# Kernel optimization log

Hardware: AMD Instinct MI355X
Metric: run time of the kernel (lower is better)

Reference implementation:

```python
import jax, jax.numpy as jnp
import numpy as np

NF = 64      # feature channels of h
K = 3        # dynamic filter spatial size (padding=1 in source implies k=3)
FACTOR = 4   # pixel-unshuffle factor


def shuffle_down(x, f):
    # torch pixel_unshuffle: (B,C,H*f,W*f) -> (B,C*f*f,H,W)
    B, C, H, W = x.shape
    x = x.reshape(B, C, H // f, f, W // f, f)
    x = x.transpose(0, 1, 3, 5, 2, 4)
    return x.reshape(B, C * f * f, H // f, W // f)


def _patches3x3(x):
    # x: (B,C,H,W) -> (B,C,9,H,W): zero-padded 3x3 neighborhoods, row-major taps,
    # identical to the identity-filter grouped conv (im2col) in the source.
    H, W = x.shape[-2], x.shape[-1]
    xp = jnp.pad(x, ((0, 0), (0, 0), (1, 1), (1, 1)))
    shifts = [xp[:, :, dy:dy + H, dx:dx + W] for dy in range(K) for dx in range(K)]
    return jnp.stack(shifts, axis=2)


def setup_inputs() -> dict:
    key = jax.random.key(0)
    k1, k2, k3, k4 = jax.random.split(key, 4)
    B, H, W = 2, 256, 256
    h = jax.random.normal(k1, (B, NF, H, W), dtype=jnp.float32)
    i_t = jax.random.normal(k2, (B, 3, H * FACTOR, W * FACTOR), dtype=jnp.float32)
    conv_w = jax.random.normal(k3, (K * K, 3 * FACTOR ** 2, K, K), dtype=jnp.float32) * 0.05
    conv_b = jax.random.normal(k4, (K * K,), dtype=jnp.float32) * 0.05
    return {"h": h, "i_t": i_t, "conv_w": conv_w, "conv_b": conv_b}


def reference(h, i_t, conv_w, conv_b):
    # predict per-pixel 3x3 filters from the shuffled-down guidance frame
    x = shuffle_down(i_t, FACTOR)  # (B, 48, H, W)
    f = jax.lax.conv_general_dilated(
        x, conv_w, window_strides=(1, 1), padding=((1, 1), (1, 1)),
        dimension_numbers=("NCHW", "OIHW", "NCHW"))
    filters = jax.nn.relu(f + conv_b[None, :, None, None])  # (B, 9, H, W)

    # dynamic per-pixel conv: same 3x3 filter applied to every channel of h
    patches = _patches3x3(h)  # (B, nf, 9, H, W)
    out = jnp.einsum("bcfhw,bfhw->bchw", patches, filters)  # (B, nf, H, W)
    return out
```

## Files before the change

### kernel.cpp

```cpp
#include <hip/hip_runtime.h>

#define TILE 16
#define HSZ 256
#define WSZ 256
#define NFC 64
#define PLANE (HSZ * WSZ)

typedef __attribute__((ext_vector_type(8))) short short8;
typedef __attribute__((ext_vector_type(4))) float f32x4;

__device__ inline unsigned short f2bf(float f) {
    unsigned u = __builtin_bit_cast(unsigned, f);
    return (unsigned short)((u + 0x7fffu + ((u >> 16) & 1u)) >> 16);
}

__global__ void prep_wfrag(const float* __restrict__ wbuf,
                           unsigned short* __restrict__ wfragG)
{
    const int kb   = blockIdx.x;
    const int lane = threadIdx.x;
    const int l15  = lane & 15;
    const int kg   = lane >> 4;
    unsigned short v8[8];
#pragma unroll
    for (int j = 0; j < 8; ++j) {
        const int k = kb * 32 + kg * 8 + j;
        float w = 0.f;
        if (k < 432 && l15 < 9) {
            const int kk = k / 48;
            const int ic = k - kk * 48;
            w = wbuf[l15 * 432 + ic * 9 + kk];
        }
        v8[j] = f2bf(w);
    }
    unsigned short* p = wfragG + (size_t)kb * 512 + lane * 8;
    *(ushort4*)(p)     = ushort4{v8[0], v8[1], v8[2], v8[3]};
    *(ushort4*)(p + 4) = ushort4{v8[4], v8[5], v8[6], v8[7]};
}

__global__ __launch_bounds__(128) void filter_conv_mfma2(
    const float* __restrict__ i_t,
    const unsigned short* __restrict__ wfragG,
    const float* __restrict__ bias,
    float* __restrict__ fbuf)
{
    __shared__ __align__(16) unsigned short xs[180 * 48];

    const int tid  = threadIdx.x;
    const int X0 = blockIdx.x * 16;
    const int Y0 = blockIdx.y * 8;
    const int b  = blockIdx.z;
    const int lane = tid & 63;
    const int l15  = tid & 15;
    const int kg   = (tid >> 4) & 3;
    const int wv   = tid >> 6;

    const float bv = (l15 < 9) ? bias[l15] : 0.f;
    const float* itb = i_t + (size_t)b * 3 * (PLANE * 16);

    {
        float4 lreg[17]; int sdst[17];
#pragma unroll
        for (int k = 0; k < 17; ++k) {
            const int v = tid + 128 * k;
            const int sp = v / 12, t = v - sp * 12;
            const int c3 = t >> 2, fy = t & 3;
            const int ly = sp / 18, lx = sp - ly * 18;
            const int Y = Y0 - 1 + ly, X = X0 - 1 + lx;
            float4 val = make_float4(0.f, 0.f, 0.f, 0.f);
            if (v < 2160 && (unsigned)Y < HSZ && (unsigned)X < WSZ)
                val = *(const float4*)(itb + ((size_t)c3 * 1024 + (4 * Y + fy)) * 1024 + 4 * X);
            lreg[k] = val;
            sdst[k] = (v < 2160) ? (sp * 48 + t * 4) : -1;
        }
#pragma unroll
        for (int k = 0; k < 17; ++k) {
            if (sdst[k] >= 0) {
                ushort4 u{f2bf(lreg[k].x), f2bf(lreg[k].y), f2bf(lreg[k].z), f2bf(lreg[k].w)};
                *(ushort4*)(xs + sdst[k]) = u;
            }
        }
    }

    short8 wf[14];
#pragma unroll
    for (int kb = 0; kb < 14; ++kb)
        wf[kb] = *(const short8*)(wfragG + (size_t)kb * 512 + lane * 8);

    __syncthreads();

    f32x4 acc0 = {0.f, 0.f, 0.f, 0.f}, acc1 = acc0, acc2 = acc0, acc3 = acc0;
#pragma unroll
    for (int kb = 0; kb < 14; ++kb) {
        const int k0 = kb * 32 + kg * 8;
        int off = 0;
        if (k0 < 432) {
            const int kk  = k0 / 48;
            const int ic0 = k0 - kk * 48;
            const int ky  = kk / 3;
            const int kx  = kk - 3 * ky;
            off = ((wv * 4 + ky) * 18 + l15 + kx) * 48 + ic0;
        }
        short8 a0 = *(const short8*)(xs + off);
        short8 a1 = *(const short8*)(xs + off + 864);
        short8 a2 = *(const short8*)(xs + off + 1728);
        short8 a3 = *(const short8*)(xs + off + 2592);
        acc0 = __builtin_amdgcn_mfma_f32_16x16x32_bf16(a0, wf[kb], acc0, 0, 0, 0);
        acc1 = __builtin_amdgcn_mfma_f32_16x16x32_bf16(a1, wf[kb], acc1, 0, 0, 0);
        acc2 = __builtin_amdgcn_mfma_f32_16x16x32_bf16(a2, wf[kb], acc2, 0, 0, 0);
        acc3 = __builtin_amdgcn_mfma_f32_16x16x32_bf16(a3, wf[kb], acc3, 0, 0, 0);
    }

    __syncthreads();
    float* lf = (float*)xs;
    if (l15 < 9) {
#pragma unroll
        for (int i = 0; i < 4; ++i) {
            const int py = wv * 4 + i;
            f32x4 A = (i == 0) ? acc0 : (i == 1) ? acc1 : (i == 2) ? acc2 : acc3;
#pragma unroll
            for (int r = 0; r < 4; ++r) {
                const int px = kg * 4 + r;
                lf[(py * 16 + px) * 12 + l15] = fmaxf(A[r] + bv, 0.f);
            }
        }
    }
    __syncthreads();
    float* fb = fbuf + (size_t)b * PLANE * 12;
#pragma unroll
    for (int k = 0; k < 3; ++k) {
        const int v = tid + 128 * k;
        const int row = v / 48, off = v - row * 48;
        *(float4*)(fb + ((size_t)(Y0 + row) * WSZ + X0) * 12 + off * 4) =
            *(const float4*)(lf + v * 4);
    }
}

__global__ __launch_bounds__(256, 4) void dyn_apply4(
    const float* __restrict__ hbuf,
    const float* __restrict__ fbuf,
    float* __restrict__ out)
{
    __shared__ __align__(16) float hs[8 * 18 * 40];

    const int tid  = threadIdx.x;
    const int pq   = tid & 7;
    const int py   = (tid >> 3) & 15;
    const int c_lo = tid >> 7;
    const int cg = blockIdx.x & 7;
    const int X0 = (blockIdx.x >> 3) * 32;
    const int Y0 = blockIdx.y * TILE;
    const int b  = blockIdx.z;

    float flt[4][9];
    {
        const float* fb = fbuf + ((size_t)b * PLANE + (size_t)(Y0 + py) * WSZ + X0 + pq * 4) * 12;
#pragma unroll
        for (int j = 0; j < 4; ++j) {
            float4 f0 = *(const float4*)(fb + j * 12);
            float4 f1 = *(const float4*)(fb + j * 12 + 4);
            float  f8 = fb[j * 12 + 8];
            flt[j][0] = f0.x; flt[j][1] = f0.y; flt[j][2] = f0.z; flt[j][3] = f0.w;
            flt[j][4] = f1.x; flt[j][5] = f1.y; flt[j][6] = f1.z; flt[j][7] = f1.w;
            flt[j][8] = f8;
        }
    }

    const float* hp = hbuf + ((size_t)b * NFC + cg * 8) * PLANE;
    {
        float rv[20]; int dst[20];
#pragma unroll
        for (int k = 0; k < 20; ++k) {
            const int v = tid + 256 * k;
            const int c = v / 612;
            const int r = v - c * 612;
            const int row = r / 34, l = r - row * 34;
            const int Y = Y0 - 1 + row;
            const int X = X0 - 1 + l;
            float val = 0.f;
            if (v < 4896 && (unsigned)Y < HSZ && (unsigned)X < WSZ)
                val = hp[(size_t)c * PLANE + (size_t)Y * WSZ + X];
            rv[k] = val;
            dst[k] = (v < 4896) ? (c * 720 + row * 40 + 3 + l) : -1;
        }
#pragma unroll
        for (int k = 0; k < 20; ++k)
            if (dst[k] >= 0) hs[dst[k]] = rv[k];
    }
    __syncthreads();

    float a[4][4];
#pragma unroll
    for (int cc = 0; cc < 4; ++cc)
#pragma unroll
        for (int j = 0; j < 4; ++j) a[cc][j] = 0.f;

#pragma unroll
    for (int cc = 0; cc < 4; ++cc) {
        const float* pl = hs + (c_lo + 2 * cc) * 720;
#pragma unroll
        for (int ky = 0; ky < 3; ++ky) {
            const float* rp = pl + (py + ky) * 40 + pq * 4;
            float4 w0 = *(const float4*)rp;
            float4 w1 = *(const float4*)(rp + 4);
            float  w8 = rp[8];
            const float vs[9] = {w0.x, w0.y, w0.z, w0.w, w1.x, w1.y, w1.z, w1.w, w8};
#pragma unroll
            for (int kx = 0; kx < 3; ++kx)
#pragma unroll
                for (int j = 0; j < 4; ++j)
                    a[cc][j] = fmaf(vs[3 + kx + j], flt[j][ky * 3 + kx], a[cc][j]);
        }
    }

#pragma unroll
    for (int cc = 0; cc < 4; ++cc) {
        const int ch = cg * 8 + c_lo + 2 * cc;
        *(float4*)(out + ((size_t)b * NFC + ch) * PLANE
                       + (size_t)(Y0 + py) * WSZ + X0 + pq * 4)
            = make_float4(a[cc][0], a[cc][1], a[cc][2], a[cc][3]);
    }
}

__global__ void filter_conv_mfma(const float* __restrict__ i_t,
                                 const float* __restrict__ wbuf,
                                 const float* __restrict__ bias,
                                 float* __restrict__ fbuf)
{
    __shared__ __align__(16) unsigned short xs[324 * 56];

    const int tid = threadIdx.x;
    const int X0 = blockIdx.x * TILE;
    const int Y0 = blockIdx.y * TILE;
    const int b  = blockIdx.z;
    const int l15 = tid & 15;
    const int kg  = (tid >> 4) & 3;
    const int wv  = tid >> 6;

    float* wsh = (float*)xs;
    for (int i = tid; i < 3888; i += 256) wsh[i] = wbuf[i];
    __syncthreads();

    short8 wfrag[14];
#pragma unroll
    for (int kb = 0; kb < 14; ++kb) {
#pragma unroll
        for (int j = 0; j < 8; ++j) {
            const int k = kb * 32 + kg * 8 + j;
            float w = 0.f;
            if (k < 432 && l15 < 9) {
                const int kk = k / 48;
                const int ic = k - kk * 48;
                w = wsh[l15 * 432 + ic * 9 + kk];
            }
            wfrag[kb][j] = (short)f2bf(w);
        }
    }
    const float bv = (l15 < 9) ? bias[l15] : 0.f;
    __syncthreads();

    const float* itb = i_t + (size_t)b * 3 * (PLANE * 16);
    for (int v = tid; v < 3888; v += 256) {
        const int sp = v / 12;
        const int t  = v - sp * 12;
        const int c3 = t >> 2, fy = t & 3;
        const int ly = sp / 18, lx = sp - ly * 18;
        const int Y = Y0 - 1 + ly, X = X0 - 1 + lx;
        float4 val = make_float4(0.f, 0.f, 0.f, 0.f);
        if (Y >= 0 && Y < HSZ && X >= 0 && X < WSZ)
            val = *(const float4*)(itb + ((size_t)c3 * 1024 + (4 * Y + fy)) * 1024 + 4 * X);
        ushort4 u;
        u.x = f2bf(val.x); u.y = f2bf(val.y); u.z = f2bf(val.z); u.w = f2bf(val.w);
        *(ushort4*)(xs + sp * 56 + t * 4) = u;
    }
    __syncthreads();

    f32x4 acc0 = {0.f, 0.f, 0.f, 0.f}, acc1 = acc0, acc2 = acc0, acc3 = acc0;
#pragma unroll
    for (int kb = 0; kb < 14; ++kb) {
        const int k0 = kb * 32 + kg * 8;
        int off = 0;
        if (k0 < 432) {
            const int kk  = k0 / 48;
            const int ic0 = k0 - kk * 48;
            const int ky  = kk / 3;
            const int kx  = kk - 3 * ky;
            off = ((wv * 4 + ky) * 18 + l15 + kx) * 56 + ic0;
        }
        short8 a0 = *(const short8*)(xs + off);
        short8 a1 = *(const short8*)(xs + off + 1008);
        short8 a2 = *(const short8*)(xs + off + 2016);
        short8 a3 = *(const short8*)(xs + off + 3024);
        acc0 = __builtin_amdgcn_mfma_f32_16x16x32_bf16(a0, wfrag[kb], acc0, 0, 0, 0);
        acc1 = __builtin_amdgcn_mfma_f32_16x16x32_bf16(a1, wfrag[kb], acc1, 0, 0, 0);
        acc2 = __builtin_amdgcn_mfma_f32_16x16x32_bf16(a2, wfrag[kb], acc2, 0, 0, 0);
        acc3 = __builtin_amdgcn_mfma_f32_16x16x32_bf16(a3, wfrag[kb], acc3, 0, 0, 0);
    }

    if (l15 < 9) {
        float* fb = fbuf + (size_t)b * PLANE * 12;
#pragma unroll
        for (int i = 0; i < 4; ++i) {
            const int py = wv * 4 + i;
            f32x4 A = (i == 0) ? acc0 : (i == 1) ? acc1 : (i == 2) ? acc2 : acc3;
#pragma unroll
            for (int r = 0; r < 4; ++r) {
                const int px = kg * 4 + r;
                fb[((size_t)(Y0 + py) * WSZ + X0 + px) * 12 + l15] = fmaxf(A[r] + bv, 0.f);
            }
        }
    }
}

__global__ __launch_bounds__(256, 2) void fused_dynfilter(
    const float* __restrict__ hbuf,
    const float* __restrict__ i_t,
    const float* __restrict__ wbuf,
    const float* __restrict__ bias,
    float* __restrict__ out)
{
    __shared__ __align__(16) float smem[15552];
    float4* xs4 = (float4*)smem;

    const int tid = threadIdx.x;
    const int px = tid & 15;
    const int py = tid >> 4;
    const int X0 = blockIdx.x * TILE;
    const int Y0 = blockIdx.y * TILE;
    const int b  = blockIdx.z;

    const float* itb = i_t + (size_t)b * 3 * 1024 * 1024;
    for (int v = tid; v < 3888; v += 256) {
        int sp = v / 12;
        int t  = v - sp * 12;
        int c3 = t >> 2, fy = t & 3;
        int ly = sp / 18, lx = sp - ly * 18;
        int Y = Y0 - 1 + ly, X = X0 - 1 + lx;
        float4 val = make_float4(0.f, 0.f, 0.f, 0.f);
        if (Y >= 0 && Y < HSZ && X >= 0 && X < WSZ)
            val = *(const float4*)(itb + ((size_t)c3 * 1024 + (4 * Y + fy)) * 1024 + 4 * X);
        xs4[t * 324 + sp] = val;
    }
    __syncthreads();

    float acc[9];
#pragma unroll
    for (int oc = 0; oc < 9; ++oc) acc[oc] = bias[oc];

#pragma unroll 1
    for (int ky = 0; ky < 3; ++ky)
#pragma unroll 1
        for (int kx = 0; kx < 3; ++kx) {
            const int sp = (py + ky) * 18 + (px + kx);
            const int kk = ky * 3 + kx;
#pragma unroll
            for (int ic4 = 0; ic4 < 12; ++ic4) {
                float4 v = xs4[ic4 * 324 + sp];
                const int chb = ((ic4 >> 2) << 4) + ((ic4 & 3) << 2);
                const float* wp = wbuf + (size_t)chb * 9 + kk;
                const float vv[4] = {v.x, v.y, v.z, v.w};
#pragma unroll
                for (int j = 0; j < 4; ++j)
#pragma unroll
                    for (int oc = 0; oc < 9; ++oc)
                        acc[oc] = fmaf(vv[j], wp[j * 9 + (size_t)oc * 432], acc[oc]);
            }
        }

    float flt[9];
#pragma unroll
    for (int oc = 0; oc < 9; ++oc) flt[oc] = fmaxf(acc[oc], 0.f);

    float4* hs4 = (float4*)smem;
#pragma unroll 1
    for (int cg = 0; cg < 16; ++cg) {
        __syncthreads();
        const float* hp = hbuf + ((size_t)b * NFC + cg * 4) * PLANE;
        for (int idx = tid; idx < 1296; idx += 256) {
            int c  = idx / 324;
            int sp = idx - c * 324;
            int ly = sp / 18, lx = sp - ly * 18;
            int Y = Y0 - 1 + ly, X = X0 - 1 + lx;
            float vv = 0.f;
            if (Y >= 0 && Y < HSZ && X >= 0 && X < WSZ)
                vv = hp[(size_t)c * PLANE + (size_t)Y * WSZ + X];
            smem[sp * 4 + c] = vv;
        }
        __syncthreads();

        float s0 = 0.f, s1 = 0.f, s2 = 0.f, s3 = 0.f;
#pragma unroll
        for (int ky = 0; ky < 3; ++ky)
#pragma unroll
            for (int kx = 0; kx < 3; ++kx) {
                float4 v = hs4[(py + ky) * 18 + (px + kx)];
                float f = flt[ky * 3 + kx];
                s0 = fmaf(v.x, f, s0);
                s1 = fmaf(v.y, f, s1);
                s2 = fmaf(v.z, f, s2);
                s3 = fmaf(v.w, f, s3);
            }
        size_t o = (((size_t)b * NFC + cg * 4) * HSZ + (Y0 + py)) * WSZ + (X0 + px);
        out[o]                     = s0;
        out[o + (size_t)PLANE]     = s1;
        out[o + (size_t)2 * PLANE] = s2;
        out[o + (size_t)3 * PLANE] = s3;
    }
}

extern "C" void kernel_launch(void* const* d_in, const int* in_sizes, int n_in,
                              void* d_out, int out_size, void* d_ws, size_t ws_size,
                              hipStream_t stream) {
    const float* h      = (const float*)d_in[0];
    const float* i_t    = (const float*)d_in[1];
    const float* conv_w = (const float*)d_in[2];
    const float* conv_b = (const float*)d_in[3];
    float* out = (float*)d_out;

    const int B = in_sizes[0] / (NFC * PLANE);
    const size_t fbuf_sz  = (size_t)B * PLANE * 12 * sizeof(float);
    const size_t wfrag_sz = 14 * 512 * sizeof(unsigned short);

    if (ws_size >= fbuf_sz + wfrag_sz) {
        float* fbuf = (float*)d_ws;
        unsigned short* wfragG = (unsigned short*)((char*)d_ws + fbuf_sz);
        prep_wfrag<<<dim3(14), 64, 0, stream>>>(conv_w, wfragG);
        dim3 g1(WSZ / 16, HSZ / 8, B);
        filter_conv_mfma2<<<g1, 128, 0, stream>>>(i_t, wfragG, conv_b, fbuf);
        dim3 g2((WSZ / 32) * 8, HSZ / TILE, B);
        dyn_apply4<<<g2, 256, 0, stream>>>(h, fbuf, out);
    } else if (ws_size >= fbuf_sz) {
        float* fbuf = (float*)d_ws;
        dim3 g1(WSZ / TILE, HSZ / TILE, B);
        filter_conv_mfma<<<g1, 256, 0, stream>>>(i_t, conv_w, conv_b, fbuf);
        dim3 g2((WSZ / 32) * 8, HSZ / TILE, B);
        dyn_apply4<<<g2, 256, 0, stream>>>(h, fbuf, out);
    } else {
        dim3 grid(WSZ / TILE, HSZ / TILE, B);
        fused_dynfilter<<<grid, 256, 0, stream>>>(h, i_t, conv_w, conv_b, out);
    }
}
```

Measured before the change: 137.7 us.

## Store filters planar, vectorize halo loads, widen filter-conv blocks to 256 threads

The intermediate filter buffer changes from a per-pixel 12-float interleaved layout to nine planar channel arrays. This shrinks it from 12 to 9 floats per pixel, so the apply kernel reads filters as float4 per channel. The apply kernel's halo load of h now uses float4 global loads with an aligned 4-float left margin instead of scalar loads. The filter conv uses 256 threads with two MFMA row tiles per wave instead of four, giving more waves per block and fewer registers per thread. It also drops the unused intermediate fallback path. The apply kernel now over-fetches some halo columns, and the filter conv writes in smaller pieces.

```diff
diff --git a/kernel.cpp b/kernel.cpp
--- a/kernel.cpp
+++ b/kernel.cpp
@@ -38,11 +38,11 @@
     *(ushort4*)(p + 4) = ushort4{v8[4], v8[5], v8[6], v8[7]};
 }
 
-__global__ __launch_bounds__(128) void filter_conv_mfma2(
+__global__ __launch_bounds__(256) void filter_conv_mfma3(
     const float* __restrict__ i_t,
     const unsigned short* __restrict__ wfragG,
     const float* __restrict__ bias,
-    float* __restrict__ fbuf)
+    float* __restrict__ fbuf, int Bn)
 {
     __shared__ __align__(16) unsigned short xs[180 * 48];
 
@@ -59,10 +59,10 @@
     const float* itb = i_t + (size_t)b * 3 * (PLANE * 16);
 
     {
-        float4 lreg[17]; int sdst[17];
-#pragma unroll
-        for (int k = 0; k < 17; ++k) {
-            const int v = tid + 128 * k;
+        float4 lreg[9]; int sdst[9];
+#pragma unroll
+        for (int k = 0; k < 9; ++k) {
+            const int v = tid + 256 * k;
             const int sp = v / 12, t = v - sp * 12;
             const int c3 = t >> 2, fy = t & 3;
             const int ly = sp / 18, lx = sp - ly * 18;
@@ -74,7 +74,7 @@
             sdst[k] = (v < 2160) ? (sp * 48 + t * 4) : -1;
         }
 #pragma unroll
-        for (int k = 0; k < 17; ++k) {
+        for (int k = 0; k < 9; ++k) {
             if (sdst[k] >= 0) {
                 ushort4 u{f2bf(lreg[k].x), f2bf(lreg[k].y), f2bf(lreg[k].z), f2bf(lreg[k].w)};
                 *(ushort4*)(xs + sdst[k]) = u;
@@ -89,7 +89,7 @@
 
     __syncthreads();
 
-    f32x4 acc0 = {0.f, 0.f, 0.f, 0.f}, acc1 = acc0, acc2 = acc0, acc3 = acc0;
+    f32x4 acc0 = {0.f, 0.f, 0.f, 0.f}, acc1 = acc0;
 #pragma unroll
     for (int kb = 0; kb < 14; ++kb) {
         const int k0 = kb * 32 + kg * 8;
@@ -99,49 +99,49 @@
             const int ic0 = k0 - kk * 48;
             const int ky  = kk / 3;
             const int kx  = kk - 3 * ky;
-            off = ((wv * 4 + ky) * 18 + l15 + kx) * 48 + ic0;
+            off = ((2 * wv + ky) * 18 + l15 + kx) * 48 + ic0;
         }
         short8 a0 = *(const short8*)(xs + off);
         short8 a1 = *(const short8*)(xs + off + 864);
-        short8 a2 = *(const short8*)(xs + off + 1728);
-        short8 a3 = *(const short8*)(xs + off + 2592);
         acc0 = __builtin_amdgcn_mfma_f32_16x16x32_bf16(a0, wf[kb], acc0, 0, 0, 0);
         acc1 = __builtin_amdgcn_mfma_f32_16x16x32_bf16(a1, wf[kb], acc1, 0, 0, 0);
-        acc2 = __builtin_amdgcn_mfma_f32_16x16x32_bf16(a2, wf[kb], acc2, 0, 0, 0);
-        acc3 = __builtin_amdgcn_mfma_f32_16x16x32_bf16(a3, wf[kb], acc3, 0, 0, 0);
     }
 
     __syncthreads();
     float* lf = (float*)xs;
     if (l15 < 9) {
 #pragma unroll
-        for (int i = 0; i < 4; ++i) {
-            const int py = wv * 4 + i;
-            f32x4 A = (i == 0) ? acc0 : (i == 1) ? acc1 : (i == 2) ? acc2 : acc3;
+        for (int t = 0; t < 2; ++t) {
+            const int py = 2 * wv + t;
+            f32x4 A = t ? acc1 : acc0;
 #pragma unroll
             for (int r = 0; r < 4; ++r) {
                 const int px = kg * 4 + r;
-                lf[(py * 16 + px) * 12 + l15] = fmaxf(A[r] + bv, 0.f);
+                lf[l15 * 128 + py * 16 + px] = fmaxf(A[r] + bv, 0.f);
             }
         }
     }
     __syncthreads();
-    float* fb = fbuf + (size_t)b * PLANE * 12;
-#pragma unroll
-    for (int k = 0; k < 3; ++k) {
-        const int v = tid + 128 * k;
-        const int row = v / 48, off = v - row * 48;
-        *(float4*)(fb + ((size_t)(Y0 + row) * WSZ + X0) * 12 + off * 4) =
-            *(const float4*)(lf + v * 4);
-    }
-}
-
-__global__ __launch_bounds__(256, 4) void dyn_apply4(
+    {
+        const int v0 = tid;
+        const int oc = v0 >> 5, rem = v0 & 31, py = rem >> 2, xf4 = rem & 3;
+        *(float4*)(fbuf + ((size_t)oc * Bn + b) * PLANE + (size_t)(Y0 + py) * WSZ + X0 + xf4 * 4)
+            = *(const float4*)(lf + oc * 128 + py * 16 + xf4 * 4);
+        if (tid < 32) {
+            const int v1 = tid + 256;
+            const int oc1 = v1 >> 5, rem1 = v1 & 31, py1 = rem1 >> 2, xf41 = rem1 & 3;
+            *(float4*)(fbuf + ((size_t)oc1 * Bn + b) * PLANE + (size_t)(Y0 + py1) * WSZ + X0 + xf41 * 4)
+                = *(const float4*)(lf + oc1 * 128 + py1 * 16 + xf41 * 4);
+        }
+    }
+}
+
+__global__ __launch_bounds__(256, 4) void dyn_apply5(
     const float* __restrict__ hbuf,
     const float* __restrict__ fbuf,
-    float* __restrict__ out)
+    float* __restrict__ out, int Bn)
 {
-    __shared__ __align__(16) float hs[8 * 18 * 40];
+    __shared__ __align__(16) float hs[8 * 720];
 
     const int tid  = threadIdx.x;
     const int pq   = tid & 7;
@@ -152,40 +152,34 @@
     const int Y0 = blockIdx.y * TILE;
     const int b  = blockIdx.z;
 
-    float flt[4][9];
+    float4 flt4[9];
     {
-        const float* fb = fbuf + ((size_t)b * PLANE + (size_t)(Y0 + py) * WSZ + X0 + pq * 4) * 12;
-#pragma unroll
-        for (int j = 0; j < 4; ++j) {
-            float4 f0 = *(const float4*)(fb + j * 12);
-            float4 f1 = *(const float4*)(fb + j * 12 + 4);
-            float  f8 = fb[j * 12 + 8];
-            flt[j][0] = f0.x; flt[j][1] = f0.y; flt[j][2] = f0.z; flt[j][3] = f0.w;
-            flt[j][4] = f1.x; flt[j][5] = f1.y; flt[j][6] = f1.z; flt[j][7] = f1.w;
-            flt[j][8] = f8;
-        }
+        const size_t pix = (size_t)b * PLANE + (size_t)(Y0 + py) * WSZ + X0 + pq * 4;
+#pragma unroll
+        for (int oc = 0; oc < 9; ++oc)
+            flt4[oc] = *(const float4*)(fbuf + (size_t)oc * Bn * PLANE + pix);
     }
 
     const float* hp = hbuf + ((size_t)b * NFC + cg * 8) * PLANE;
     {
-        float rv[20]; int dst[20];
-#pragma unroll
-        for (int k = 0; k < 20; ++k) {
+        float4 rv[6]; int dst[6];
+#pragma unroll
+        for (int k = 0; k < 6; ++k) {
             const int v = tid + 256 * k;
-            const int c = v / 612;
-            const int r = v - c * 612;
-            const int row = r / 34, l = r - row * 34;
-            const int Y = Y0 - 1 + row;
-            const int X = X0 - 1 + l;
-            float val = 0.f;
-            if (v < 4896 && (unsigned)Y < HSZ && (unsigned)X < WSZ)
-                val = hp[(size_t)c * PLANE + (size_t)Y * WSZ + X];
+            const int c = v / 180;
+            const int r = v - c * 180;
+            const int row = r / 10, xq = r - row * 10;
+            const int Y  = Y0 - 1 + row;
+            const int X4 = X0 - 4 + xq * 4;
+            float4 val = make_float4(0.f, 0.f, 0.f, 0.f);
+            if (v < 1440 && (unsigned)Y < HSZ && (unsigned)X4 < WSZ)
+                val = *(const float4*)(hp + (size_t)c * PLANE + (size_t)Y * WSZ + X4);
             rv[k] = val;
-            dst[k] = (v < 4896) ? (c * 720 + row * 40 + 3 + l) : -1;
-        }
-#pragma unroll
-        for (int k = 0; k < 20; ++k)
-            if (dst[k] >= 0) hs[dst[k]] = rv[k];
+            dst[k] = (v < 1440) ? (c * 720 + row * 40 + xq * 4) : -1;
+        }
+#pragma unroll
+        for (int k = 0; k < 6; ++k)
+            if (dst[k] >= 0) *(float4*)(hs + dst[k]) = rv[k];
     }
     __syncthreads();
 
@@ -209,7 +203,7 @@
             for (int kx = 0; kx < 3; ++kx)
 #pragma unroll
                 for (int j = 0; j < 4; ++j)
-                    a[cc][j] = fmaf(vs[3 + kx + j], flt[j][ky * 3 + kx], a[cc][j]);
+                    a[cc][j] = fmaf(vs[3 + kx + j], flt4[ky * 3 + kx][j], a[cc][j]);
         }
     }
 
@@ -219,96 +213,6 @@
         *(float4*)(out + ((size_t)b * NFC + ch) * PLANE
                        + (size_t)(Y0 + py) * WSZ + X0 + pq * 4)
             = make_float4(a[cc][0], a[cc][1], a[cc][2], a[cc][3]);
-    }
-}
-
-__global__ void filter_conv_mfma(const float* __restrict__ i_t,
-                                 const float* __restrict__ wbuf,
-                                 const float* __restrict__ bias,
-                                 float* __restrict__ fbuf)
-{
-    __shared__ __align__(16) unsigned short xs[324 * 56];
-
-    const int tid = threadIdx.x;
-    const int X0 = blockIdx.x * TILE;
-    const int Y0 = blockIdx.y * TILE;
-    const int b  = blockIdx.z;
-    const int l15 = tid & 15;
-    const int kg  = (tid >> 4) & 3;
-    const int wv  = tid >> 6;
-
-    float* wsh = (float*)xs;
-    for (int i = tid; i < 3888; i += 256) wsh[i] = wbuf[i];
-    __syncthreads();
-
-    short8 wfrag[14];
-#pragma unroll
-    for (int kb = 0; kb < 14; ++kb) {
-#pragma unroll
-        for (int j = 0; j < 8; ++j) {
-            const int k = kb * 32 + kg * 8 + j;
-            float w = 0.f;
-            if (k < 432 && l15 < 9) {
-                const int kk = k / 48;
-                const int ic = k - kk * 48;
-                w = wsh[l15 * 432 + ic * 9 + kk];
-            }
-            wfrag[kb][j] = (short)f2bf(w);
-        }
-    }
-    const float bv = (l15 < 9) ? bias[l15] : 0.f;
-    __syncthreads();
-
-    const float* itb = i_t + (size_t)b * 3 * (PLANE * 16);
-    for (int v = tid; v < 3888; v += 256) {
-        const int sp = v / 12;
-        const int t  = v - sp * 12;
-        const int c3 = t >> 2, fy = t & 3;
-        const int ly = sp / 18, lx = sp - ly * 18;
-        const int Y = Y0 - 1 + ly, X = X0 - 1 + lx;
-        float4 val = make_float4(0.f, 0.f, 0.f, 0.f);
-        if (Y >= 0 && Y < HSZ && X >= 0 && X < WSZ)
-            val = *(const float4*)(itb + ((size_t)c3 * 1024 + (4 * Y + fy)) * 1024 + 4 * X);
-        ushort4 u;
-        u.x = f2bf(val.x); u.y = f2bf(val.y); u.z = f2bf(val.z); u.w = f2bf(val.w);
-        *(ushort4*)(xs + sp * 56 + t * 4) = u;
-    }
-    __syncthreads();
-
-    f32x4 acc0 = {0.f, 0.f, 0.f, 0.f}, acc1 = acc0, acc2 = acc0, acc3 = acc0;
-#pragma unroll
-    for (int kb = 0; kb < 14; ++kb) {
-        const int k0 = kb * 32 + kg * 8;
-        int off = 0;
-        if (k0 < 432) {
-            const int kk  = k0 / 48;
-            const int ic0 = k0 - kk * 48;
-            const int ky  = kk / 3;
-            const int kx  = kk - 3 * ky;
-            off = ((wv * 4 + ky) * 18 + l15 + kx) * 56 + ic0;
-        }
-        short8 a0 = *(const short8*)(xs + off);
-        short8 a1 = *(const short8*)(xs + off + 1008);
-        short8 a2 = *(const short8*)(xs + off + 2016);
-        short8 a3 = *(const short8*)(xs + off + 3024);
-        acc0 = __builtin_amdgcn_mfma_f32_16x16x32_bf16(a0, wfrag[kb], acc0, 0, 0, 0);
-        acc1 = __builtin_amdgcn_mfma_f32_16x16x32_bf16(a1, wfrag[kb], acc1, 0, 0, 0);
-        acc2 = __builtin_amdgcn_mfma_f32_16x16x32_bf16(a2, wfrag[kb], acc2, 0, 0, 0);
-        acc3 = __builtin_amdgcn_mfma_f32_16x16x32_bf16(a3, wfrag[kb], acc3, 0, 0, 0);
-    }
-
-    if (l15 < 9) {
-        float* fb = fbuf + (size_t)b * PLANE * 12;
-#pragma unroll
-        for (int i = 0; i < 4; ++i) {
-            const int py = wv * 4 + i;
-            f32x4 A = (i == 0) ? acc0 : (i == 1) ? acc1 : (i == 2) ? acc2 : acc3;
-#pragma unroll
-            for (int r = 0; r < 4; ++r) {
-                const int px = kg * 4 + r;
-                fb[((size_t)(Y0 + py) * WSZ + X0 + px) * 12 + l15] = fmaxf(A[r] + bv, 0.f);
-            }
-        }
     }
 }
 
@@ -418,7 +322,7 @@
     float* out = (float*)d_out;
 
     const int B = in_sizes[0] / (NFC * PLANE);
-    const size_t fbuf_sz  = (size_t)B * PLANE * 12 * sizeof(float);
+    const size_t fbuf_sz  = (size_t)9 * B * PLANE * sizeof(float);
     const size_t wfrag_sz = 14 * 512 * sizeof(unsigned short);
 
     if (ws_size >= fbuf_sz + wfrag_sz) {
@@ -426,15 +330,9 @@
         unsigned short* wfragG = (unsigned short*)((char*)d_ws + fbuf_sz);
         prep_wfrag<<<dim3(14), 64, 0, stream>>>(conv_w, wfragG);
         dim3 g1(WSZ / 16, HSZ / 8, B);
-        filter_conv_mfma2<<<g1, 128, 0, stream>>>(i_t, wfragG, conv_b, fbuf);
+        filter_conv_mfma3<<<g1, 256, 0, stream>>>(i_t, wfragG, conv_b, fbuf, B);
         dim3 g2((WSZ / 32) * 8, HSZ / TILE, B);
-        dyn_apply4<<<g2, 256, 0, stream>>>(h, fbuf, out);
-    } else if (ws_size >= fbuf_sz) {
-        float* fbuf = (float*)d_ws;
-        dim3 g1(WSZ / TILE, HSZ / TILE, B);
-        filter_conv_mfma<<<g1, 256, 0, stream>>>(i_t, conv_w, conv_b, fbuf);
-        dim3 g2((WSZ / 32) * 8, HSZ / TILE, B);
-        dyn_apply4<<<g2, 256, 0, stream>>>(h, fbuf, out);
+        dyn_apply5<<<g2, 256, 0, stream>>>(h, fbuf, out, B);
     } else {
         dim3 grid(WSZ / TILE, HSZ / TILE, B);
         fused_dynfilter<<<grid, 256, 0, stream>>>(h, i_t, conv_w, conv_b, out);
```

Result: faster. 125.7 us (-8.7%).
